# Kernel tuning notes

Measured on AMD Instinct MI355X. Metric: run time of the kernel, lower is better.

Reference implementation:

```python
import jax, jax.numpy as jnp
import numpy as np

N_NODES = 100000
N_EDGES = 1600000
D_IN = 64
D_OUT = 64
BN_EPS = 1e-5


def setup_inputs() -> dict:
    key = jax.random.key(0)
    k_x, k_src, k_dst, k_ew, k_w = jax.random.split(key, 5)
    x = jax.random.normal(k_x, (N_NODES, D_IN), dtype=jnp.float32)
    edge_src = jax.random.randint(k_src, (N_EDGES,), 0, N_NODES, dtype=jnp.int32)
    edge_dst = jax.random.randint(k_dst, (N_EDGES,), 0, N_NODES, dtype=jnp.int32)
    edge_weight = jax.random.uniform(k_ew, (N_EDGES,), dtype=jnp.float32)
    # Xavier-uniform weight, zero bias (reset_parameters)
    limit = float(np.sqrt(6.0 / (D_IN + D_OUT)))
    W = jax.random.uniform(k_w, (D_IN, D_OUT), dtype=jnp.float32, minval=-limit, maxval=limit)
    bias = jnp.zeros((D_OUT,), dtype=jnp.float32)
    gamma = jnp.ones((D_OUT,), dtype=jnp.float32)
    beta = jnp.zeros((D_OUT,), dtype=jnp.float32)
    return {"x": x, "edge_src": edge_src, "edge_dst": edge_dst,
            "edge_weight": edge_weight, "W": W, "bias": bias,
            "gamma": gamma, "beta": beta}


def reference(x, edge_src, edge_dst, edge_weight, W, bias, gamma, beta):
    # GraphConvolution: support = x @ W  -> [N, D_OUT]
    support = jnp.matmul(x, W)
    # spmm(adj, support) with adj in COO form: out[d] += w_e * support[s]
    msgs = edge_weight[:, None] * support[edge_src]        # [E, D_OUT]
    agg = jax.ops.segment_sum(msgs, edge_dst, num_segments=N_NODES)
    out = agg + bias
    # BatchNorm1d (training mode: batch statistics over node dim)
    mean = jnp.mean(out, axis=0)
    var = jnp.var(out, axis=0)
    out = (out - mean) * jax.lax.rsqrt(var + BN_EPS) * gamma + beta
    # ReLU activation; dropout is identity in deterministic/inference mode
    return jax.nn.relu(out)
```

## Files before the change

kernel.cpp:

```cpp
#include <hip/hip_runtime.h>
#include <hip/hip_bf16.h>

#define NN 100000
#define NE 1600000
#define DD 64
#define NCOARSE 392
#define GEMM_TILES 1563
#define PLACE_EPB 4096
#define PLACE_BLOCKS 392
#define CAP 4736

__device__ inline unsigned short f2bf(float f) {
    __hip_bfloat16 h = __float2bfloat16(f);
    unsigned short s; __builtin_memcpy(&s, &h, 2); return s;
}

__global__ __launch_bounds__(512) void k_zero(int* __restrict__ gcnt) {
    if (threadIdx.x < NCOARSE) gcnt[threadIdx.x] = 0;
}

__global__ __launch_bounds__(256) void k_gemm_scatter(const float* __restrict__ x,
                                                      const float* __restrict__ Wg,
                                                      unsigned* __restrict__ support2,
                                                      const int* __restrict__ esrc,
                                                      const int* __restrict__ edst,
                                                      const float* __restrict__ ew,
                                                      int* __restrict__ gcnt,
                                                      int2* __restrict__ permA) {
    if (blockIdx.x < PLACE_BLOCKS) {
        const int blk = blockIdx.x;
        __shared__ int h[NCOARSE];
        __shared__ int loff[NCOARSE];
        for (int i = threadIdx.x; i < NCOARSE; i += 256) h[i] = 0;
        __syncthreads();
        const int e0 = blk * PLACE_EPB;
#pragma unroll 4
        for (int k = 0; k < 16; ++k) {
            const int e = e0 + k * 256 + threadIdx.x;
            if (e < NE) atomicAdd(&h[edst[e] >> 8], 1);
        }
        __syncthreads();
        for (int i = threadIdx.x; i < NCOARSE; i += 256) {
            const int hc = h[i];
            loff[i] = i * CAP + ((hc > 0) ? atomicAdd(&gcnt[i], hc) : 0);
        }
        __syncthreads();
#pragma unroll 4
        for (int k = 0; k < 16; ++k) {
            const int e = e0 + k * 256 + threadIdx.x;
            if (e < NE) {
                const int d = edst[e];
                const int c = d >> 8;
                const int p = atomicAdd(&loff[c], 1);
                if (p < c * CAP + CAP)
                    permA[p] = make_int2(esrc[e] | ((d & 255) << 17), __float_as_int(ew[e]));
            }
        }
        return;
    }

    __shared__ float Xs[64 * DD];
    const int r0 = (blockIdx.x - PLACE_BLOCKS) * 64;
    const int nrows = (r0 + 64 <= NN) ? 64 : (NN - r0);
    const int t = threadIdx.x;

    const float4* xg = (const float4*)(x + (size_t)r0 * DD);
    for (int i = t; i < nrows * 16; i += 256) {
        const int row = i >> 4, k4 = i & 15;
        *(float4*)&Xs[row * 64 + ((k4 ^ (row & 15)) << 2)] = xg[i];
    }
    if (nrows < 64) {
        for (int i = nrows * 16 + t; i < 64 * 16; i += 256)
            ((float4*)Xs)[i] = make_float4(0.f, 0.f, 0.f, 0.f);
    }
    __syncthreads();

    const int lane = t & 63;
    const int w = __builtin_amdgcn_readfirstlane(t >> 6);
    const float* Wp = Wg + w * 16;

    float acc[16];
#pragma unroll
    for (int c = 0; c < 16; ++c) acc[c] = 0.f;

#pragma unroll 4
    for (int k4 = 0; k4 < 16; ++k4) {
        const float4 xv = *(const float4*)&Xs[lane * 64 + ((k4 ^ (lane & 15)) << 2)];
        const float* wr = Wp + k4 * 4 * DD;
#pragma unroll
        for (int c = 0; c < 16; ++c) {
            acc[c] = fmaf(xv.x, wr[c],          acc[c]);
            acc[c] = fmaf(xv.y, wr[DD + c],     acc[c]);
            acc[c] = fmaf(xv.z, wr[2 * DD + c], acc[c]);
            acc[c] = fmaf(xv.w, wr[3 * DD + c], acc[c]);
        }
    }

    __syncthreads();
    unsigned* Us = (unsigned*)Xs;
#pragma unroll
    for (int j = 0; j < 8; ++j) {
        const unsigned p = (unsigned)f2bf(acc[2 * j]) |
                           ((unsigned)f2bf(acc[2 * j + 1]) << 16);
        const int cp = 8 * w + j;
        Us[lane * 32 + ((cp + lane) & 31)] = p;
    }
    __syncthreads();
    uint4* sg = (uint4*)(support2 + (size_t)r0 * 32);
#pragma unroll
    for (int it = 0; it < 2; ++it) {
        const int g4 = t + it * 256;
        const int row = g4 >> 3, c0 = (g4 & 7) << 2;
        if (row < nrows) {
            uint4 v;
            v.x = Us[row * 32 + ((c0 + 0 + row) & 31)];
            v.y = Us[row * 32 + ((c0 + 1 + row) & 31)];
            v.z = Us[row * 32 + ((c0 + 2 + row) & 31)];
            v.w = Us[row * 32 + ((c0 + 3 + row) & 31)];
            sg[g4] = v;
        }
    }
}

__global__ __launch_bounds__(1024, 8) void k_sortgather(const int* __restrict__ gcnt,
                                                        const int2* __restrict__ permA,
                                                        const uint4* __restrict__ support4,
                                                        float* __restrict__ out,
                                                        float* __restrict__ pstat) {
    __shared__ int2 eL[CAP];
    __shared__ unsigned short idx16[CAP];
    __shared__ int cnt[256], st[257], cur[256], wtot[4];
    __shared__ float red[16][128];

    const int c = blockIdx.x, t = threadIdx.x;
    const int cs = c * CAP;
    const int sz = min(gcnt[c], CAP);
    const int wave = t >> 6, lane = t & 63;

    for (int j = t; j < sz; j += 1024) eL[j] = permA[cs + j];
    if (t < 256) cnt[t] = 0;
    __syncthreads();

    for (int j = t; j < sz; j += 1024)
        atomicAdd(&cnt[(eL[j].x >> 17) & 255], 1);
    __syncthreads();

    int v = 0, xv = 0;
    if (wave < 4) {
        v = cnt[t]; xv = v;
#pragma unroll
        for (int o = 1; o < 64; o <<= 1) {
            int u = __shfl_up(xv, o, 64);
            if (lane >= o) xv += u;
        }
        if (lane == 63) wtot[wave] = xv;
    }
    __syncthreads();
    if (t < 4) {
        int w0 = wtot[t], xw = w0;
#pragma unroll
        for (int o = 1; o < 4; o <<= 1) {
            int u = __shfl_up(xw, o, 64);
            if (t >= o) xw += u;
        }
        wtot[t] = xw - w0;
    }
    __syncthreads();
    if (wave < 4) {
        const int base = wtot[wave] + xv - v;
        st[t] = base;
        cur[t] = base;
    }
    if (t == 0) st[256] = sz;
    __syncthreads();

    for (int j = t; j < sz; j += 1024) {
        int p = atomicAdd(&cur[(eL[j].x >> 17) & 255], 1);
        idx16[p] = (unsigned short)j;
    }
    __syncthreads();

    const int sub = lane >> 3, q = lane & 7;
    const int node0 = c * 256;
    float sacc[8] = {0.f, 0.f, 0.f, 0.f, 0.f, 0.f, 0.f, 0.f};
    float sqacc[8] = {0.f, 0.f, 0.f, 0.f, 0.f, 0.f, 0.f, 0.f};
    for (int n = wave; n < 256; n += 16) {
        const int bs = st[n], be = st[n + 1];
        float acc[8] = {0.f, 0.f, 0.f, 0.f, 0.f, 0.f, 0.f, 0.f};
        for (int j0 = bs; j0 < be; j0 += 8) {
            const int j = j0 + sub;
            if (j < be) {
                const int2 m = eL[idx16[j]];
                const uint4 p = support4[(size_t)(m.x & 0x1FFFF) * 8 + q];
                const float w = __int_as_float(m.y);
                acc[0] = fmaf(w, __uint_as_float(p.x << 16), acc[0]);
                acc[1] = fmaf(w, __uint_as_float(p.x & 0xffff0000u), acc[1]);
                acc[2] = fmaf(w, __uint_as_float(p.y << 16), acc[2]);
                acc[3] = fmaf(w, __uint_as_float(p.y & 0xffff0000u), acc[3]);
                acc[4] = fmaf(w, __uint_as_float(p.z << 16), acc[4]);
                acc[5] = fmaf(w, __uint_as_float(p.z & 0xffff0000u), acc[5]);
                acc[6] = fmaf(w, __uint_as_float(p.w << 16), acc[6]);
                acc[7] = fmaf(w, __uint_as_float(p.w & 0xffff0000u), acc[7]);
            }
        }
#pragma unroll
        for (int i = 0; i < 8; ++i) {
            acc[i] += __shfl_xor(acc[i], 8, 64);
            acc[i] += __shfl_xor(acc[i], 16, 64);
            acc[i] += __shfl_xor(acc[i], 32, 64);
        }
        const int node = node0 + n;
        if (sub == 0 && node < NN) {
            float* op = out + (size_t)node * DD + q * 8;
            *(float4*)op = make_float4(acc[0], acc[1], acc[2], acc[3]);
            *(float4*)(op + 4) = make_float4(acc[4], acc[5], acc[6], acc[7]);
#pragma unroll
            for (int k = 0; k < 8; ++k) {
                sacc[k] += acc[k];
                sqacc[k] = fmaf(acc[k], acc[k], sqacc[k]);
            }
        }
    }

    if (sub == 0) {
#pragma unroll
        for (int k = 0; k < 8; ++k) {
            red[wave][q * 8 + k] = sacc[k];
            red[wave][64 + q * 8 + k] = sqacc[k];
        }
    }
    __syncthreads();
    if (t < 128) {
        float a = 0.f;
#pragma unroll
        for (int wv = 0; wv < 16; ++wv) a += red[wv][t];
        pstat[c * 128 + t] = a;
    }
}

__global__ __launch_bounds__(256) void k_finalstats(const float* __restrict__ pstat,
                                                    const float* __restrict__ gamma,
                                                    const float* __restrict__ beta,
                                                    float* __restrict__ out) {
    __shared__ float red[128];
    __shared__ float ssl[128];
    const int t = threadIdx.x;
    if (t < 128) {
        float acc = 0.f;
        for (int b = 0; b < NCOARSE; ++b)
            acc += pstat[b * 128 + t];
        red[t] = acc;
    }
    __syncthreads();
    if (t < DD) {
        const float invn = 1.0f / NN;
        const float mean = red[t] * invn;
        const float var = fmaxf(red[DD + t] * invn - mean * mean, 0.f);
        const float sc = rsqrtf(var + 1e-5f) * gamma[t];
        ssl[t] = sc;
        ssl[DD + t] = beta[t] - mean * sc;
    }
    __syncthreads();

    float4* out4 = (float4*)out;
    const int total4 = NN * DD / 4;
    for (int i = blockIdx.x * 256 + t; i < total4; i += 256 * 256) {
        const int c = (i & 15) << 2;
        float4 v = out4[i];
        float4 o;
        o.x = fmaxf(fmaf(v.x, ssl[c + 0], ssl[DD + c + 0]), 0.f);
        o.y = fmaxf(fmaf(v.y, ssl[c + 1], ssl[DD + c + 1]), 0.f);
        o.z = fmaxf(fmaf(v.z, ssl[c + 2], ssl[DD + c + 2]), 0.f);
        o.w = fmaxf(fmaf(v.w, ssl[c + 3], ssl[DD + c + 3]), 0.f);
        out4[i] = o;
    }
}

extern "C" void kernel_launch(void* const* d_in, const int* in_sizes, int n_in,
                              void* d_out, int out_size, void* d_ws, size_t ws_size,
                              hipStream_t stream) {
    const float* x     = (const float*)d_in[0];
    const int*   esrc  = (const int*)d_in[1];
    const int*   edst  = (const int*)d_in[2];
    const float* ew    = (const float*)d_in[3];
    const float* W     = (const float*)d_in[4];
    const float* gamma = (const float*)d_in[6];
    const float* beta  = (const float*)d_in[7];
    float*       out   = (float*)d_out;

    char* ws = (char*)d_ws;
    unsigned* support2 = (unsigned*)ws;  ws += (size_t)NN * DD * 2;
    int2*     permA  = (int2*)ws;     ws += (size_t)NCOARSE * CAP * 8;
    int*   gcnt   = (int*)ws;    ws += NCOARSE * 4;
    float* pstat  = (float*)ws;  ws += (size_t)NCOARSE * 128 * 4;

    k_zero        <<<1, 512, 0, stream>>>(gcnt);
    k_gemm_scatter<<<PLACE_BLOCKS + GEMM_TILES, 256, 0, stream>>>(
                      x, W, support2, esrc, edst, ew, gcnt, permA);
    k_sortgather  <<<NCOARSE, 1024, 0, stream>>>(gcnt, permA,
                      (const uint4*)support2, out, pstat);
    k_finalstats  <<<256, 256, 0, stream>>>(pstat, gamma, beta, out);
}
```

Measured before the change: 203.4 us.

## Halve coarse bucket size and reduce BN stats with global atomics

Destination buckets now cover 128 nodes instead of 256, which doubles the sort-gather blocks to 784 with 512 threads each and shrinks the per-block LDS edge buffer. This should improve load balance and occupancy across CUs. Per-block partial statistics are now added straight into a global 128-float array with atomics, so the final kernel no longer has to serially reduce several hundred partials. The trade-off is that float atomics make the statistics order-nondeterministic, and the smaller per-bucket capacity raises the risk of overflow and dropped edges.

```diff
diff --git a/kernel.cpp b/kernel.cpp
--- a/kernel.cpp
+++ b/kernel.cpp
@@ -4,19 +4,21 @@
 #define NN 100000
 #define NE 1600000
 #define DD 64
-#define NCOARSE 392
+#define NB 784
 #define GEMM_TILES 1563
 #define PLACE_EPB 4096
 #define PLACE_BLOCKS 392
-#define CAP 4736
+#define CAP 2560
 
 __device__ inline unsigned short f2bf(float f) {
     __hip_bfloat16 h = __float2bfloat16(f);
     unsigned short s; __builtin_memcpy(&s, &h, 2); return s;
 }
 
-__global__ __launch_bounds__(512) void k_zero(int* __restrict__ gcnt) {
-    if (threadIdx.x < NCOARSE) gcnt[threadIdx.x] = 0;
+__global__ __launch_bounds__(1024) void k_zero(int* __restrict__ gcnt,
+                                               float* __restrict__ gstat) {
+    if (threadIdx.x < NB) gcnt[threadIdx.x] = 0;
+    if (threadIdx.x < 128) gstat[threadIdx.x] = 0.f;
 }
 
 __global__ __launch_bounds__(256) void k_gemm_scatter(const float* __restrict__ x,
@@ -29,18 +31,18 @@
                                                       int2* __restrict__ permA) {
     if (blockIdx.x < PLACE_BLOCKS) {
         const int blk = blockIdx.x;
-        __shared__ int h[NCOARSE];
-        __shared__ int loff[NCOARSE];
-        for (int i = threadIdx.x; i < NCOARSE; i += 256) h[i] = 0;
+        __shared__ int h[NB];
+        __shared__ int loff[NB];
+        for (int i = threadIdx.x; i < NB; i += 256) h[i] = 0;
         __syncthreads();
         const int e0 = blk * PLACE_EPB;
 #pragma unroll 4
         for (int k = 0; k < 16; ++k) {
             const int e = e0 + k * 256 + threadIdx.x;
-            if (e < NE) atomicAdd(&h[edst[e] >> 8], 1);
+            if (e < NE) atomicAdd(&h[edst[e] >> 7], 1);
         }
         __syncthreads();
-        for (int i = threadIdx.x; i < NCOARSE; i += 256) {
+        for (int i = threadIdx.x; i < NB; i += 256) {
             const int hc = h[i];
             loff[i] = i * CAP + ((hc > 0) ? atomicAdd(&gcnt[i], hc) : 0);
         }
@@ -50,10 +52,10 @@
             const int e = e0 + k * 256 + threadIdx.x;
             if (e < NE) {
                 const int d = edst[e];
-                const int c = d >> 8;
+                const int c = d >> 7;
                 const int p = atomicAdd(&loff[c], 1);
                 if (p < c * CAP + CAP)
-                    permA[p] = make_int2(esrc[e] | ((d & 255) << 17), __float_as_int(ew[e]));
+                    permA[p] = make_int2(esrc[e] | ((d & 127) << 17), __float_as_int(ew[e]));
             }
         }
         return;
@@ -122,69 +124,60 @@
     }
 }
 
-__global__ __launch_bounds__(1024, 8) void k_sortgather(const int* __restrict__ gcnt,
-                                                        const int2* __restrict__ permA,
-                                                        const uint4* __restrict__ support4,
-                                                        float* __restrict__ out,
-                                                        float* __restrict__ pstat) {
+__global__ __launch_bounds__(512, 8) void k_sortgather(const int* __restrict__ gcnt,
+                                                       const int2* __restrict__ permA,
+                                                       const uint4* __restrict__ support4,
+                                                       float* __restrict__ out,
+                                                       float* __restrict__ gstat) {
     __shared__ int2 eL[CAP];
     __shared__ unsigned short idx16[CAP];
-    __shared__ int cnt[256], st[257], cur[256], wtot[4];
-    __shared__ float red[16][128];
+    __shared__ int cnt[128], st[129], cur[128];
+    __shared__ int wtot0;
+    __shared__ float red[8][128];
 
     const int c = blockIdx.x, t = threadIdx.x;
     const int cs = c * CAP;
     const int sz = min(gcnt[c], CAP);
     const int wave = t >> 6, lane = t & 63;
 
-    for (int j = t; j < sz; j += 1024) eL[j] = permA[cs + j];
-    if (t < 256) cnt[t] = 0;
-    __syncthreads();
-
-    for (int j = t; j < sz; j += 1024)
-        atomicAdd(&cnt[(eL[j].x >> 17) & 255], 1);
+    for (int j = t; j < sz; j += 512) eL[j] = permA[cs + j];
+    if (t < 128) cnt[t] = 0;
+    __syncthreads();
+
+    for (int j = t; j < sz; j += 512)
+        atomicAdd(&cnt[(eL[j].x >> 17) & 127], 1);
     __syncthreads();
 
     int v = 0, xv = 0;
-    if (wave < 4) {
+    if (t < 128) {
         v = cnt[t]; xv = v;
 #pragma unroll
         for (int o = 1; o < 64; o <<= 1) {
             int u = __shfl_up(xv, o, 64);
             if (lane >= o) xv += u;
         }
-        if (lane == 63) wtot[wave] = xv;
-    }
-    __syncthreads();
-    if (t < 4) {
-        int w0 = wtot[t], xw = w0;
-#pragma unroll
-        for (int o = 1; o < 4; o <<= 1) {
-            int u = __shfl_up(xw, o, 64);
-            if (t >= o) xw += u;
-        }
-        wtot[t] = xw - w0;
-    }
-    __syncthreads();
-    if (wave < 4) {
-        const int base = wtot[wave] + xv - v;
+        if (t == 63) wtot0 = xv;
+    }
+    __syncthreads();
+    if (t < 128) {
+        const int base = ((t >= 64) ? wtot0 : 0) + xv - v;
         st[t] = base;
         cur[t] = base;
     }
-    if (t == 0) st[256] = sz;
-    __syncthreads();
-
-    for (int j = t; j < sz; j += 1024) {
-        int p = atomicAdd(&cur[(eL[j].x >> 17) & 255], 1);
+    if (t == 0) st[128] = sz;
+    __syncthreads();
+
+    for (int j = t; j < sz; j += 512) {
+        int p = atomicAdd(&cur[(eL[j].x >> 17) & 127], 1);
         idx16[p] = (unsigned short)j;
     }
     __syncthreads();
 
     const int sub = lane >> 3, q = lane & 7;
-    const int node0 = c * 256;
+    const int node0 = c * 128;
     float sacc[8] = {0.f, 0.f, 0.f, 0.f, 0.f, 0.f, 0.f, 0.f};
     float sqacc[8] = {0.f, 0.f, 0.f, 0.f, 0.f, 0.f, 0.f, 0.f};
-    for (int n = wave; n < 256; n += 16) {
+    for (int n = wave; n < 128; n += 8) {
         const int bs = st[n], be = st[n + 1];
         float acc[8] = {0.f, 0.f, 0.f, 0.f, 0.f, 0.f, 0.f, 0.f};
         for (int j0 = bs; j0 < be; j0 += 8) {
@@ -233,29 +226,21 @@
     if (t < 128) {
         float a = 0.f;
 #pragma unroll
-        for (int wv = 0; wv < 16; ++wv) a += red[wv][t];
-        pstat[c * 128 + t] = a;
-    }
-}
-
-__global__ __launch_bounds__(256) void k_finalstats(const float* __restrict__ pstat,
+        for (int wv = 0; wv < 8; ++wv) a += red[wv][t];
+        atomicAdd(&gstat[t], a);
+    }
+}
+
+__global__ __launch_bounds__(256) void k_finalstats(const float* __restrict__ gstat,
                                                     const float* __restrict__ gamma,
                                                     const float* __restrict__ beta,
                                                     float* __restrict__ out) {
-    __shared__ float red[128];
     __shared__ float ssl[128];
     const int t = threadIdx.x;
-    if (t < 128) {
-        float acc = 0.f;
-        for (int b = 0; b < NCOARSE; ++b)
-            acc += pstat[b * 128 + t];
-        red[t] = acc;
-    }
-    __syncthreads();
     if (t < DD) {
         const float invn = 1.0f / NN;
-        const float mean = red[t] * invn;
-        const float var = fmaxf(red[DD + t] * invn - mean * mean, 0.f);
+        const float mean = gstat[t] * invn;
+        const float var = fmaxf(gstat[DD + t] * invn - mean * mean, 0.f);
         const float sc = rsqrtf(var + 1e-5f) * gamma[t];
         ssl[t] = sc;
         ssl[DD + t] = beta[t] - mean * sc;
@@ -290,14 +275,14 @@
 
     char* ws = (char*)d_ws;
     unsigned* support2 = (unsigned*)ws;  ws += (size_t)NN * DD * 2;
-    int2*     permA  = (int2*)ws;     ws += (size_t)NCOARSE * CAP * 8;
-    int*   gcnt   = (int*)ws;    ws += NCOARSE * 4;
-    float* pstat  = (float*)ws;  ws += (size_t)NCOARSE * 128 * 4;
-
-    k_zero        <<<1, 512, 0, stream>>>(gcnt);
+    int2*     permA  = (int2*)ws;     ws += (size_t)NB * CAP * 8;
+    int*   gcnt   = (int*)ws;    ws += NB * 4;
+    float* gstat  = (float*)ws;  ws += 128 * 4;
+
+    k_zero        <<<1, 1024, 0, stream>>>(gcnt, gstat);
     k_gemm_scatter<<<PLACE_BLOCKS + GEMM_TILES, 256, 0, stream>>>(
                       x, W, support2, esrc, edst, ew, gcnt, permA);
-    k_sortgather  <<<NCOARSE, 1024, 0, stream>>>(gcnt, permA,
-                      (const uint4*)support2, out, pstat);
-    k_finalstats  <<<256, 256, 0, stream>>>(pstat, gamma, beta, out);
-}
+    k_sortgather  <<<NB, 512, 0, stream>>>(gcnt, permA,
+                      (const uint4*)support2, out, gstat);
+    k_finalstats  <<<256, 256, 0, stream>>>(gstat, gamma, beta, out);
+}
```

Result: no change. 199.5 us (-1.9%).

## Scatter edges directly into sorted LDS buffer and reduce stats with global atomics

Applied to the files above, without the earlier changes.

The sort-gather kernel no longer stages the coarse bucket into LDS and then keeps a 16-bit index permutation. It reads permA from global memory twice (once for the histogram, once for placement) and writes the edge records straight into a sorted LDS array, which removes one indirection in the gather loop and the idx16 buffer. Per-block BN partial statistics are now accumulated with global float atomics into a 128-entry buffer zeroed in k_zero. This removes the serial 392-way reduction from every block of k_finalstats, at the cost of nondeterministic summation order.

```diff
diff --git a/kernel.cpp b/kernel.cpp
--- a/kernel.cpp
+++ b/kernel.cpp
@@ -15,8 +15,10 @@
     unsigned short s; __builtin_memcpy(&s, &h, 2); return s;
 }
 
-__global__ __launch_bounds__(512) void k_zero(int* __restrict__ gcnt) {
+__global__ __launch_bounds__(512) void k_zero(int* __restrict__ gcnt,
+                                              float* __restrict__ gstat) {
     if (threadIdx.x < NCOARSE) gcnt[threadIdx.x] = 0;
+    if (threadIdx.x < 128) gstat[threadIdx.x] = 0.f;
 }
 
 __global__ __launch_bounds__(256) void k_gemm_scatter(const float* __restrict__ x,
@@ -126,9 +128,8 @@
                                                         const int2* __restrict__ permA,
                                                         const uint4* __restrict__ support4,
                                                         float* __restrict__ out,
-                                                        float* __restrict__ pstat) {
-    __shared__ int2 eL[CAP];
-    __shared__ unsigned short idx16[CAP];
+                                                        float* __restrict__ gstat) {
+    __shared__ int2 eS[CAP];
     __shared__ int cnt[256], st[257], cur[256], wtot[4];
     __shared__ float red[16][128];
 
@@ -137,12 +138,11 @@
     const int sz = min(gcnt[c], CAP);
     const int wave = t >> 6, lane = t & 63;
 
-    for (int j = t; j < sz; j += 1024) eL[j] = permA[cs + j];
     if (t < 256) cnt[t] = 0;
     __syncthreads();
 
     for (int j = t; j < sz; j += 1024)
-        atomicAdd(&cnt[(eL[j].x >> 17) & 255], 1);
+        atomicAdd(&cnt[(permA[cs + j].x >> 17) & 255], 1);
     __syncthreads();
 
     int v = 0, xv = 0;
@@ -175,8 +175,9 @@
     __syncthreads();
 
     for (int j = t; j < sz; j += 1024) {
-        int p = atomicAdd(&cur[(eL[j].x >> 17) & 255], 1);
-        idx16[p] = (unsigned short)j;
+        const int2 m = permA[cs + j];
+        const int p = atomicAdd(&cur[(m.x >> 17) & 255], 1);
+        eS[p] = m;
     }
     __syncthreads();
 
@@ -190,7 +191,7 @@
         for (int j0 = bs; j0 < be; j0 += 8) {
             const int j = j0 + sub;
             if (j < be) {
-                const int2 m = eL[idx16[j]];
+                const int2 m = eS[j];
                 const uint4 p = support4[(size_t)(m.x & 0x1FFFF) * 8 + q];
                 const float w = __int_as_float(m.y);
                 acc[0] = fmaf(w, __uint_as_float(p.x << 16), acc[0]);
@@ -234,28 +235,20 @@
         float a = 0.f;
 #pragma unroll
         for (int wv = 0; wv < 16; ++wv) a += red[wv][t];
-        pstat[c * 128 + t] = a;
-    }
-}
-
-__global__ __launch_bounds__(256) void k_finalstats(const float* __restrict__ pstat,
+        atomicAdd(&gstat[t], a);
+    }
+}
+
+__global__ __launch_bounds__(256) void k_finalstats(const float* __restrict__ gstat,
                                                     const float* __restrict__ gamma,
                                                     const float* __restrict__ beta,
                                                     float* __restrict__ out) {
-    __shared__ float red[128];
     __shared__ float ssl[128];
     const int t = threadIdx.x;
-    if (t < 128) {
-        float acc = 0.f;
-        for (int b = 0; b < NCOARSE; ++b)
-            acc += pstat[b * 128 + t];
-        red[t] = acc;
-    }
-    __syncthreads();
     if (t < DD) {
         const float invn = 1.0f / NN;
-        const float mean = red[t] * invn;
-        const float var = fmaxf(red[DD + t] * invn - mean * mean, 0.f);
+        const float mean = gstat[t] * invn;
+        const float var = fmaxf(gstat[DD + t] * invn - mean * mean, 0.f);
         const float sc = rsqrtf(var + 1e-5f) * gamma[t];
         ssl[t] = sc;
         ssl[DD + t] = beta[t] - mean * sc;
@@ -292,12 +285,12 @@
     unsigned* support2 = (unsigned*)ws;  ws += (size_t)NN * DD * 2;
     int2*     permA  = (int2*)ws;     ws += (size_t)NCOARSE * CAP * 8;
     int*   gcnt   = (int*)ws;    ws += NCOARSE * 4;
-    float* pstat  = (float*)ws;  ws += (size_t)NCOARSE * 128 * 4;
-
-    k_zero        <<<1, 512, 0, stream>>>(gcnt);
+    float* gstat  = (float*)ws;  ws += 128 * 4;
+
+    k_zero        <<<1, 512, 0, stream>>>(gcnt, gstat);
     k_gemm_scatter<<<PLACE_BLOCKS + GEMM_TILES, 256, 0, stream>>>(
                       x, W, support2, esrc, edst, ew, gcnt, permA);
     k_sortgather  <<<NCOARSE, 1024, 0, stream>>>(gcnt, permA,
-                      (const uint4*)support2, out, pstat);
-    k_finalstats  <<<256, 256, 0, stream>>>(pstat, gamma, beta, out);
-}
+                      (const uint4*)support2, out, gstat);
+    k_finalstats  <<<256, 256, 0, stream>>>(gstat, gamma, beta, out);
+}
```

New measurement: 197.2 us. -3.1%, faster.
